# Optimization experiments

Measured on AMD Instinct MI355X. Metric: run time of the kernel, lower is better.

The kernel has to match this reference:

```python
import jax, jax.numpy as jnp
import numpy as np

B = 2048
GIN = 128      # gating input features
GH = 128       # gating hidden units
E = 8          # experts
XIN = 512      # expert input features
U = 512        # expert layer units
OUT = 512      # expert output features


def setup_inputs() -> dict:
    key = jax.random.key(0)
    ks = jax.random.split(key, 16)
    rn = lambda k, shape: (jax.random.normal(k, shape) * 0.05).astype(jnp.float32)
    return {
        "gating_input": jax.random.normal(ks[0], (B, GIN), dtype=jnp.float32),
        "expert_input": jax.random.normal(ks[1], (B, XIN), dtype=jnp.float32),
        # gating MLP params (Dense stores kernel as (in, out))
        "Wg0": rn(ks[2], (GIN, GH)), "bg0": rn(ks[3], (GH,)),
        "Wg1": rn(ks[4], (GH, GH)), "bg1": rn(ks[5], (GH,)),
        "Wgo": rn(ks[6], (GH, E)),  "bgo": rn(ks[7], (E,)),
        # expert weight pools: alpha (E, units, in), beta (E, units)
        "alpha0": rn(ks[8], (E, U, XIN)), "beta0": rn(ks[9], (E, U)),
        "alpha1": rn(ks[10], (E, U, U)),  "beta1": rn(ks[11], (E, U)),
        "alpha2": rn(ks[12], (E, OUT, U)), "beta2": rn(ks[13], (E, OUT)),
    }


def dense_expert(x, g, alpha, beta):
    # Mathematically: (sum_e g[b,e] * alpha[e]) @ x[b] + sum_e g[b,e]*beta[e]
    # Contract input with each expert first (avoids the (B,U,I) blended-weight tensor).
    per_expert = jnp.einsum("bi,eui->beu", x, alpha)   # (B, E, U)
    w = jnp.einsum("be,beu->bu", g, per_expert)         # (B, U)
    b = jnp.einsum("be,eu->bu", g, beta)                # (B, U)
    return w + b


def reference(gating_input, expert_input, Wg0, bg0, Wg1, bg1, Wgo, bgo,
              alpha0, beta0, alpha1, beta1, alpha2, beta2):
    # Gating network: Dense+ELU x2 (dropout is identity at inference), Dense+softmax
    h = jax.nn.elu(gating_input @ Wg0 + bg0)
    h = jax.nn.elu(h @ Wg1 + bg1)
    g = jax.nn.softmax(h @ Wgo + bgo, axis=-1)          # (B, E)

    # Expert network: DenseExpert + ELU x2, final DenseExpert
    x = jax.nn.elu(dense_expert(expert_input, g, alpha0, beta0))
    x = jax.nn.elu(dense_expert(x, g, alpha1, beta1))
    y = dense_expert(x, g, alpha2, beta2)               # (B, OUT)
    return y
```

## Files before the change

### kernel.cpp

```cpp
#include <hip/hip_runtime.h>
#include <math.h>

#define BATCH 2048
#define GIN 128
#define GH 128
#define NE 8
#define XIN 512
#define UU 512

typedef __attribute__((ext_vector_type(8))) short short8;
typedef __attribute__((ext_vector_type(4))) float f32x4;

__device__ inline unsigned short f2bf(float f) {
    unsigned u = __float_as_uint(f);
    u += 0x7fffu + ((u >> 16) & 1u);
    return (unsigned short)(u >> 16);
}

__device__ inline float elu1(float x) { return x > 0.f ? x : (expf(x) - 1.f); }

__global__ __launch_bounds__(256) void gating_kernel(
    const float* __restrict__ gin, const float* __restrict__ W0, const float* __restrict__ b0,
    const float* __restrict__ W1, const float* __restrict__ b1,
    const float* __restrict__ Wo, const float* __restrict__ bo,
    float* __restrict__ g)
{
    __shared__ float xs[4][128];
    __shared__ float hs[4][128];
    __shared__ float ps[2][4][128];
    __shared__ float lp[8][4][8];
    __shared__ float ls[4][8];

    const int t = threadIdx.x;
    const int c = t & 127;
    const int h = t >> 7;
    const int row0 = blockIdx.x * 4;

    ((float*)xs)[t]       = gin[row0 * GIN + t];
    ((float*)xs)[t + 256] = gin[row0 * GIN + t + 256];
    __syncthreads();

    {
        float acc0 = 0.f, acc1 = 0.f, acc2 = 0.f, acc3 = 0.f;
        const float* Wc = W0 + c;
        #pragma unroll 8
        for (int i = h * 64; i < h * 64 + 64; ++i) {
            float w = Wc[i * GH];
            acc0 += xs[0][i] * w; acc1 += xs[1][i] * w;
            acc2 += xs[2][i] * w; acc3 += xs[3][i] * w;
        }
        ps[h][0][c] = acc0; ps[h][1][c] = acc1; ps[h][2][c] = acc2; ps[h][3][c] = acc3;
    }
    __syncthreads();
    {
        int o = t, r = o >> 7, cc = o & 127;
        hs[r][cc] = elu1(ps[0][r][cc] + ps[1][r][cc] + b0[cc]);
        o = t + 256; r = o >> 7; cc = o & 127;
        hs[r][cc] = elu1(ps[0][r][cc] + ps[1][r][cc] + b0[cc]);
    }
    __syncthreads();

    {
        float acc0 = 0.f, acc1 = 0.f, acc2 = 0.f, acc3 = 0.f;
        const float* Wc = W1 + c;
        #pragma unroll 8
        for (int i = h * 64; i < h * 64 + 64; ++i) {
            float w = Wc[i * GH];
            acc0 += hs[0][i] * w; acc1 += hs[1][i] * w;
            acc2 += hs[2][i] * w; acc3 += hs[3][i] * w;
        }
        ps[h][0][c] = acc0; ps[h][1][c] = acc1; ps[h][2][c] = acc2; ps[h][3][c] = acc3;
    }
    __syncthreads();
    {
        int o = t, r = o >> 7, cc = o & 127;
        xs[r][cc] = elu1(ps[0][r][cc] + ps[1][r][cc] + b1[cc]);
        o = t + 256; r = o >> 7; cc = o & 127;
        xs[r][cc] = elu1(ps[0][r][cc] + ps[1][r][cc] + b1[cc]);
    }
    __syncthreads();

    {
        const int e = t & 7, r = (t >> 3) & 3, q = t >> 5;
        float s = 0.f;
        #pragma unroll
        for (int i = q * 16; i < q * 16 + 16; ++i) s += xs[r][i] * Wo[i * NE + e];
        lp[q][r][e] = s;
    }
    __syncthreads();
    if (t < 32) {
        const int r = t >> 3, e = t & 7;
        float s = bo[e];
        #pragma unroll
        for (int q = 0; q < 8; ++q) s += lp[q][r][e];
        ls[r][e] = s;
    }
    __syncthreads();
    if (t < 4) {
        float mx = ls[t][0];
        #pragma unroll
        for (int e = 1; e < 8; ++e) mx = fmaxf(mx, ls[t][e]);
        float s = 0.f, ex[8];
        #pragma unroll
        for (int e = 0; e < 8; ++e) { ex[e] = expf(ls[t][e] - mx); s += ex[e]; }
        float inv = 1.f / s;
        #pragma unroll
        for (int e = 0; e < 8; ++e) g[(row0 + t) * NE + e] = ex[e] * inv;
    }
}

__global__ __launch_bounds__(256) void convert_kernel(
    const float* __restrict__ a0, const float* __restrict__ a1, const float* __restrict__ a2,
    const float* __restrict__ xv, unsigned short* __restrict__ dst)
{
    const long long vi = (long long)(blockIdx.x * blockDim.x + threadIdx.x) * 4;
    const int sel = (int)(vi >> 21);
    const float* src = (sel == 0) ? a0 : (sel == 1) ? a1 : (sel == 2) ? a2 : xv;
    float4 v = *(const float4*)(src + (vi & ((1 << 21) - 1)));
    union { unsigned short us[4]; uint2 u2; } p;
    p.us[0] = f2bf(v.x); p.us[1] = f2bf(v.y); p.us[2] = f2bf(v.z); p.us[3] = f2bf(v.w);
    *(uint2*)(dst + vi) = p.u2;
}

__global__ __launch_bounds__(256) void moe_fused_kernel(
    const unsigned short* __restrict__ A,
    const unsigned short* __restrict__ Bw,
    const float* __restrict__ g,
    const float* __restrict__ beta,
    unsigned short* __restrict__ Xnext,
    float* __restrict__ out, int last)
{
    constexpr int K = XIN;
    __shared__ unsigned short As[64 * 64];
    __shared__ unsigned short Bs[8 * 32 * 64];
    __shared__ float gs[64][8];
    __shared__ float bt[8][32];

    const int t = threadIdx.x;
    const int n0 = blockIdx.x * 32;
    const int m0 = blockIdx.y * 64;
    const int wave = t >> 6, lane = t & 63;
    const int wm = (wave >> 1) * 32;
    const int wn = (wave & 1) * 16;

    ((float2*)gs)[t] = ((const float2*)(g + (size_t)m0 * NE))[t];
    bt[t >> 5][t & 31] = beta[(t >> 5) * UU + n0 + (t & 31)];

    f32x4 acc[8][2] = {};

    const int trow = t >> 3;
    const int tcol = (t & 7) * 8;

    const unsigned short* Ae = A + (size_t)m0 * K;

    for (int ki = 0; ki < K; ki += 64) {
        __syncthreads();
        #pragma unroll
        for (int it = 0; it < 2; ++it) {
            const unsigned short* ga = Ae + (size_t)(trow + it * 32) * K + ki + tcol;
            __builtin_amdgcn_global_load_lds(
                (const __attribute__((address_space(1))) void*)ga,
                (__attribute__((address_space(3))) void*)(As + it * 2048 + t * 8), 16, 0, 0);
        }
        #pragma unroll
        for (int it = 0; it < 8; ++it) {
            const int rowflat = trow + it * 32;
            const unsigned short* gb = Bw +
                ((size_t)(rowflat >> 5) * UU + n0 + (rowflat & 31)) * K + ki + tcol;
            __builtin_amdgcn_global_load_lds(
                (const __attribute__((address_space(1))) void*)gb,
                (__attribute__((address_space(3))) void*)(Bs + it * 2048 + t * 8), 16, 0, 0);
        }
        __syncthreads();

        #pragma unroll
        for (int kk = 0; kk < 64; kk += 32) {
            short8 af[2], bf[8];
            const int fr = lane & 15;
            const int fk = kk + (lane >> 4) * 8;
            af[0] = *(const short8*)(As + (wm + fr) * 64 + fk);
            af[1] = *(const short8*)(As + (wm + fr + 16) * 64 + fk);
            #pragma unroll
            for (int e = 0; e < 8; ++e)
                bf[e] = *(const short8*)(Bs + (e * 32 + wn + fr) * 64 + fk);
            #pragma unroll
            for (int e = 0; e < 8; ++e) {
                acc[e][0] = __builtin_amdgcn_mfma_f32_16x16x32_bf16(af[0], bf[e], acc[e][0], 0, 0, 0);
                acc[e][1] = __builtin_amdgcn_mfma_f32_16x16x32_bf16(af[1], bf[e], acc[e][1], 0, 0, 0);
            }
        }
    }

    const int cl = lane & 15, rq = lane >> 4;
    const int col = n0 + wn + cl;
    #pragma unroll
    for (int i = 0; i < 2; ++i)
        #pragma unroll
        for (int r = 0; r < 4; ++r) {
            const int rl = wm + i * 16 + rq * 4 + r;
            float v = 0.f;
            #pragma unroll
            for (int e = 0; e < 8; ++e)
                v += gs[rl][e] * (acc[e][i][r] + bt[e][wn + cl]);
            if (last) out[(size_t)(m0 + rl) * UU + col] = v;
            else      Xnext[(size_t)(m0 + rl) * UU + col] = f2bf(elu1(v));
        }
}

extern "C" void kernel_launch(void* const* d_in, const int* in_sizes, int n_in,
                              void* d_out, int out_size, void* d_ws, size_t ws_size,
                              hipStream_t stream)
{
    (void)in_sizes; (void)n_in; (void)out_size; (void)ws_size;
    const float* gin = (const float*)d_in[0];
    const float* xin = (const float*)d_in[1];
    const float* W0  = (const float*)d_in[2];
    const float* b0  = (const float*)d_in[3];
    const float* W1  = (const float*)d_in[4];
    const float* b1  = (const float*)d_in[5];
    const float* Wo  = (const float*)d_in[6];
    const float* bo  = (const float*)d_in[7];
    const float* alpha[3] = {(const float*)d_in[8],  (const float*)d_in[10], (const float*)d_in[12]};
    const float* beta[3]  = {(const float*)d_in[9],  (const float*)d_in[11], (const float*)d_in[13]};
    float* out = (float*)d_out;

    char* ws = (char*)d_ws;
    float* g = (float*)ws;
    size_t off = 65536;
    unsigned short* ab = (unsigned short*)(ws + off);
    off += (size_t)3 * (1 << 21) * 2;
    unsigned short* Xb0 = (unsigned short*)(ws + off);
    off += (size_t)BATCH * XIN * 2;
    unsigned short* Xb1 = (unsigned short*)(ws + off);
    off += (size_t)BATCH * XIN * 2;

    gating_kernel<<<BATCH / 4, 256, 0, stream>>>(gin, W0, b0, W1, b1, Wo, bo, g);
    convert_kernel<<<(3 * (1 << 21) + BATCH * XIN) / 4 / 256, 256, 0, stream>>>(
        alpha[0], alpha[1], alpha[2], xin, ab);

    unsigned short* Xsrc = Xb0;
    unsigned short* Xdst = Xb1;
    for (int l = 0; l < 3; ++l) {
        moe_fused_kernel<<<dim3(UU / 32, BATCH / 64), 256, 0, stream>>>(
            Xsrc, ab + (size_t)l * (1 << 21), g, beta[l], Xdst, out, l == 2 ? 1 : 0);
        unsigned short* tmp = Xsrc; Xsrc = Xdst; Xdst = tmp;
    }
}
```

Before: 157.4 us.

## Double-buffer LDS tiles, split experts across waves, swizzle LDS to avoid bank conflicts

Restructures the MoE GEMM main loop to use a double-buffered K=32 LDS pipeline, so global-to-LDS loads of the next tile overlap MFMA work on the current one and only one barrier is needed per step. Each wave now owns two experts over the full 64x32 tile instead of all eight experts on a quarter tile. The per-expert gated sums are then reduced across waves through LDS, which allows vectorized output stores. LDS addresses are XOR-swizzled to cut bank conflicts. The cost is an extra LDS reduction pass and synchronization in the epilogue, plus more loop iterations at half the K depth.

```diff
diff --git a/kernel.cpp b/kernel.cpp
--- a/kernel.cpp
+++ b/kernel.cpp
@@ -10,6 +10,9 @@
 
 typedef __attribute__((ext_vector_type(8))) short short8;
 typedef __attribute__((ext_vector_type(4))) float f32x4;
+
+#define AS1 __attribute__((address_space(1)))
+#define AS3 __attribute__((address_space(3)))
 
 __device__ inline unsigned short f2bf(float f) {
     unsigned u = __float_as_uint(f);
@@ -131,8 +134,8 @@
     float* __restrict__ out, int last)
 {
     constexpr int K = XIN;
-    __shared__ unsigned short As[64 * 64];
-    __shared__ unsigned short Bs[8 * 32 * 64];
+    __shared__ unsigned short As[2][64 * 32];
+    __shared__ unsigned short Bs[2][8 * 32 * 32];
     __shared__ float gs[64][8];
     __shared__ float bt[8][32];
 
@@ -140,71 +143,121 @@
     const int n0 = blockIdx.x * 32;
     const int m0 = blockIdx.y * 64;
     const int wave = t >> 6, lane = t & 63;
-    const int wm = (wave >> 1) * 32;
-    const int wn = (wave & 1) * 16;
+    const int e0 = 2 * wave;
 
     ((float2*)gs)[t] = ((const float2*)(g + (size_t)m0 * NE))[t];
     bt[t >> 5][t & 31] = beta[(t >> 5) * UU + n0 + (t & 31)];
 
-    f32x4 acc[8][2] = {};
-
-    const int trow = t >> 3;
-    const int tcol = (t & 7) * 8;
-
-    const unsigned short* Ae = A + (size_t)m0 * K;
-
-    for (int ki = 0; ki < K; ki += 64) {
+    f32x4 acc[2][4][2] = {};
+
+    const int slot = t & 3;
+    const int arow = t >> 2;
+    const int acol = ((slot ^ ((arow >> 1) & 3)) * 8);
+    const unsigned short* a_src = A + (size_t)(m0 + arow) * K + acol;
+
+    const unsigned short* b_src[4];
+    #pragma unroll
+    for (int it = 0; it < 4; ++it) {
+        const int rowflat = it * 64 + arow;
+        const int bcol = ((slot ^ ((rowflat >> 1) & 3)) * 8);
+        b_src[it] = Bw + ((size_t)(rowflat >> 5) * UU + n0 + (rowflat & 31)) * K + bcol;
+    }
+
+#define STAGE(bi, ki)                                                        \
+    do {                                                                     \
+        __builtin_amdgcn_global_load_lds(                                    \
+            (const AS1 void*)(a_src + (ki)),                                 \
+            (AS3 void*)(&As[bi][t * 8]), 16, 0, 0);                          \
+        _Pragma("unroll")                                                    \
+        for (int it_ = 0; it_ < 4; ++it_)                                    \
+            __builtin_amdgcn_global_load_lds(                                \
+                (const AS1 void*)(b_src[it_] + (ki)),                        \
+                (AS3 void*)(&Bs[bi][it_ * 2048 + t * 8]), 16, 0, 0);         \
+    } while (0)
+
+#define COMPUTE(bi)                                                          \
+    do {                                                                     \
+        const int fr_ = lane & 15;                                           \
+        const int fkb_ = (lane >> 4) * 16;                                   \
+        short8 af_[4], bf_[2][2];                                            \
+        _Pragma("unroll")                                                    \
+        for (int i = 0; i < 4; ++i) {                                        \
+            const int row_ = fr_ + i * 16;                                   \
+            af_[i] = *(const short8*)((const char*)(&As[bi][0]) +            \
+                     ((row_ * 64 + fkb_) ^ (((row_ >> 1) & 3) << 4)));       \
+        }                                                                    \
+        _Pragma("unroll")                                                    \
+        for (int ep = 0; ep < 2; ++ep)                                       \
+            _Pragma("unroll")                                                \
+            for (int j = 0; j < 2; ++j) {                                    \
+                const int row_ = (e0 + ep) * 32 + j * 16 + fr_;              \
+                bf_[ep][j] = *(const short8*)((const char*)(&Bs[bi][0]) +    \
+                     ((row_ * 64 + fkb_) ^ (((row_ >> 1) & 3) << 4)));       \
+            }                                                                \
+        _Pragma("unroll")                                                    \
+        for (int ep = 0; ep < 2; ++ep)                                       \
+            _Pragma("unroll")                                                \
+            for (int i = 0; i < 4; ++i)                                      \
+                _Pragma("unroll")                                            \
+                for (int j = 0; j < 2; ++j)                                  \
+                    acc[ep][i][j] = __builtin_amdgcn_mfma_f32_16x16x32_bf16( \
+                        af_[i], bf_[ep][j], acc[ep][i][j], 0, 0, 0);         \
+    } while (0)
+
+    STAGE(0, 0);
+    __syncthreads();
+
+    for (int step = 0; step < 15; ++step) {
+        const int cur = step & 1;
+        STAGE(cur ^ 1, (step + 1) * 32);
+        COMPUTE(cur);
         __syncthreads();
-        #pragma unroll
-        for (int it = 0; it < 2; ++it) {
-            const unsigned short* ga = Ae + (size_t)(trow + it * 32) * K + ki + tcol;
-            __builtin_amdgcn_global_load_lds(
-                (const __attribute__((address_space(1))) void*)ga,
-                (__attribute__((address_space(3))) void*)(As + it * 2048 + t * 8), 16, 0, 0);
+    }
+    COMPUTE(1);
+
+    __syncthreads();
+    float* red = (float*)&Bs[0][0];
+
+    const int cl = lane & 15, rq = lane >> 4;
+    #pragma unroll
+    for (int i = 0; i < 4; ++i)
+        #pragma unroll
+        for (int j = 0; j < 2; ++j)
+            #pragma unroll
+            for (int r = 0; r < 4; ++r) {
+                const int rl = i * 16 + rq * 4 + r;
+                const int co = j * 16 + cl;
+                const float v =
+                    gs[rl][e0]     * (acc[0][i][j][r] + bt[e0][co]) +
+                    gs[rl][e0 + 1] * (acc[1][i][j][r] + bt[e0 + 1][co]);
+                red[wave * 2048 + rl * 32 + co] = v;
+            }
+    __syncthreads();
+
+    {
+        const int rl = t >> 2;
+        const int c0 = (t & 3) * 8;
+        float v[8];
+        #pragma unroll
+        for (int u = 0; u < 8; ++u) {
+            const int idx = rl * 32 + c0 + u;
+            v[u] = red[idx] + red[2048 + idx] + red[4096 + idx] + red[6144 + idx];
         }
-        #pragma unroll
-        for (int it = 0; it < 8; ++it) {
-            const int rowflat = trow + it * 32;
-            const unsigned short* gb = Bw +
-                ((size_t)(rowflat >> 5) * UU + n0 + (rowflat & 31)) * K + ki + tcol;
-            __builtin_amdgcn_global_load_lds(
-                (const __attribute__((address_space(1))) void*)gb,
-                (__attribute__((address_space(3))) void*)(Bs + it * 2048 + t * 8), 16, 0, 0);
+        if (last) {
+            float4 o0 = {v[0], v[1], v[2], v[3]};
+            float4 o1 = {v[4], v[5], v[6], v[7]};
+            float* op = out + (size_t)(m0 + rl) * UU + n0 + c0;
+            *(float4*)op = o0;
+            *(float4*)(op + 4) = o1;
+        } else {
+            union { unsigned short us[8]; short8 s8; } p;
+            #pragma unroll
+            for (int u = 0; u < 8; ++u) p.us[u] = f2bf(elu1(v[u]));
+            *(short8*)(Xnext + (size_t)(m0 + rl) * UU + n0 + c0) = p.s8;
         }
-        __syncthreads();
-
-        #pragma unroll
-        for (int kk = 0; kk < 64; kk += 32) {
-            short8 af[2], bf[8];
-            const int fr = lane & 15;
-            const int fk = kk + (lane >> 4) * 8;
-            af[0] = *(const short8*)(As + (wm + fr) * 64 + fk);
-            af[1] = *(const short8*)(As + (wm + fr + 16) * 64 + fk);
-            #pragma unroll
-            for (int e = 0; e < 8; ++e)
-                bf[e] = *(const short8*)(Bs + (e * 32 + wn + fr) * 64 + fk);
-            #pragma unroll
-            for (int e = 0; e < 8; ++e) {
-                acc[e][0] = __builtin_amdgcn_mfma_f32_16x16x32_bf16(af[0], bf[e], acc[e][0], 0, 0, 0);
-                acc[e][1] = __builtin_amdgcn_mfma_f32_16x16x32_bf16(af[1], bf[e], acc[e][1], 0, 0, 0);
-            }
-        }
-    }
-
-    const int cl = lane & 15, rq = lane >> 4;
-    const int col = n0 + wn + cl;
-    #pragma unroll
-    for (int i = 0; i < 2; ++i)
-        #pragma unroll
-        for (int r = 0; r < 4; ++r) {
-            const int rl = wm + i * 16 + rq * 4 + r;
-            float v = 0.f;
-            #pragma unroll
-            for (int e = 0; e < 8; ++e)
-                v += gs[rl][e] * (acc[e][i][r] + bt[e][wn + cl]);
-            if (last) out[(size_t)(m0 + rl) * UU + col] = v;
-            else      Xnext[(size_t)(m0 + rl) * UU + col] = f2bf(elu1(v));
-        }
+    }
+#undef STAGE
+#undef COMPUTE
 }
 
 extern "C" void kernel_launch(void* const* d_in, const int* in_sizes, int n_in,
```

New measurement: 153.2 us. -2.6%, faster.
